# Optimization experiments

Measured on AMD Instinct MI355X. Metric: run time of the kernel, lower is better.

The kernel has to match this reference:

```python
import jax, jax.numpy as jnp
import numpy as np

N_FFT = 512
HOP = 256
HID = 512
VOCAB = 44
NB_BINS = 257  # n_fft//2 + 1, == max_bin
NEG = -100000.0
POS = 200000.0


def _hann(n):
    # torch.hann_window is periodic: 0.5*(1-cos(2*pi*k/N))
    return 0.5 * (1.0 - jnp.cos(2.0 * jnp.pi * jnp.arange(n, dtype=jnp.float32) / n))


def _stft_mag(x):
    # x: (B, C, T) -> (frames, B, C(mono=1), bins), magnitude spectrogram (power=1, mono mean)
    B, C, T = x.shape
    nfr = 1 + (T - N_FFT) // HOP
    idx = jnp.arange(nfr)[:, None] * HOP + jnp.arange(N_FFT)[None, :]
    frames = x.reshape(B * C, T)[:, idx] * _hann(N_FFT)      # (BC, F, n_fft)
    mag = jnp.abs(jnp.fft.rfft(frames, axis=-1))             # (BC, F, bins)
    mag = mag.reshape(B, C, nfr, N_FFT // 2 + 1).mean(axis=1, keepdims=True)
    return mag.transpose(2, 0, 1, 3)                          # (F, B, 1, bins)


def _lstm(x, wih, whh, b, reverse):
    # x: (T, B, in). torch gate order i, f, g, o. Returns hidden states (T, B, H).
    Bt, H = x.shape[1], whh.shape[1]
    def step(carry, xt):
        h, c = carry
        g = xt @ wih.T + h @ whh.T + b
        i, f, gg, o = jnp.split(g, 4, axis=-1)
        c = jax.nn.sigmoid(f) * c + jax.nn.sigmoid(i) * jnp.tanh(gg)
        h = jax.nn.sigmoid(o) * jnp.tanh(c)
        return (h, c), h
    init = (jnp.zeros((Bt, H), x.dtype), jnp.zeros((Bt, H), x.dtype))
    _, hs = jax.lax.scan(step, init, x, reverse=reverse)
    return hs


def _bilstm(x, wih, whh, b):
    # wih: (2, 4H, in) [fwd, bwd]
    hf = _lstm(x, wih[0], whh[0], b[0], False)
    hb = _lstm(x, wih[1], whh[1], b[1], True)
    return jnp.concatenate([hf, hb], axis=-1)


def _bn(x, g, b):
    # BatchNorm1d in training mode: batch statistics over axis 0, eps=1e-5
    mu = x.mean(0)
    v = ((x - mu) ** 2).mean(0)
    return g * (x - mu) * jax.lax.rsqrt(v + 1e-5) + b


def _dtw(scores):
    # dtw[n,m] = scores[n-1,m-1] + max(dtw[n-1,m], dtw[n-1,m-1]); row-wise scan
    B, N, M = scores.shape
    row0 = jnp.full((B, M + 1), NEG, scores.dtype).at[:, 0].set(POS)
    negcol = jnp.full((B, 1), NEG, scores.dtype)
    def step(prev, s):  # prev: (B, M+1), s: (B, M)
        shifted = jnp.concatenate([negcol, prev[:, :-1]], axis=1)
        new = jnp.concatenate([negcol, s + jnp.maximum(prev, shifted)[:, 1:]], axis=1)
        return new, new[:, 1:]
    _, rows = jax.lax.scan(step, row0, scores.transpose(1, 0, 2))  # (N, B, M)
    return rows.transpose(1, 0, 2)


def setup_inputs() -> dict:
    key = jax.random.key(0)
    ks = jax.random.split(key, 10)
    B, T, L = 8, 524544, 512
    s = 0.05
    H2 = HID // 2  # per-direction hidden = 256
    return {
        "x_audio": jax.random.normal(ks[0], (B, 1, T), jnp.float32),
        "text_idx": jax.random.randint(ks[1], (B, L), 0, VOCAB),
        "txt_wih": jax.random.normal(ks[2], (2, 4 * H2, VOCAB), jnp.float32) * s,
        "txt_whh": jax.random.normal(ks[3], (2, 4 * H2, H2), jnp.float32) * s,
        "txt_b": jax.random.normal(ks[4], (2, 4 * H2), jnp.float32) * s,
        "w_s": jax.random.normal(ks[5], (HID, HID), jnp.float32) / np.sqrt(HID).astype(np.float32),
        "fc1_w": jax.random.normal(ks[6], (HID, NB_BINS), jnp.float32) * s,
        "bn1_g": jnp.ones((HID,), jnp.float32),
        "bn1_b": jnp.zeros((HID,), jnp.float32),
        "input_mean": jnp.zeros((NB_BINS,), jnp.float32),
        "input_scale": jnp.ones((NB_BINS,), jnp.float32),
        "ae_wih": jax.random.normal(ks[7], (2, 2, 4 * H2, HID), jnp.float32) * s,
        "ae_whh": jax.random.normal(ks[8], (2, 2, 4 * H2, H2), jnp.float32) * s,
        "ae_b": jax.random.normal(ks[9], (2, 2, 4 * H2), jnp.float32) * s,
    }


def reference(x_audio, text_idx, txt_wih, txt_whh, txt_b, w_s, fc1_w, bn1_g, bn1_b,
              input_mean, input_scale, ae_wih, ae_whh, ae_b):
    mag = _stft_mag(x_audio)                 # (F, B, 1, bins)
    nfr, B, C, _ = mag.shape
    # text encoder (batch_first LSTM -> time-major internally)
    oneh = jax.nn.one_hot(text_idx, VOCAB, dtype=mag.dtype)           # (B, L, V)
    h = _bilstm(oneh.transpose(1, 0, 2), txt_wih, txt_whh, txt_b)     # (L, B, HID)
    h = h.transpose(1, 0, 2)                                          # (B, L, HID)
    # audio front-end
    x = (mag[..., :NB_BINS] + input_mean) * input_scale
    x = x.reshape(nfr * B, C * NB_BINS) @ fc1_w.T
    x = jnp.tanh(_bn(x, bn1_g, bn1_b)).reshape(nfr, B, HID)
    # 2-layer bidirectional audio encoder LSTM (dropout inactive / eval)
    for l in range(2):
        x = _bilstm(x, ae_wih[l], ae_whh[l], ae_b[l])
    x = x.transpose(1, 0, 2)                                          # (B, F, HID)
    side = jnp.einsum('hk,blk->bhl', w_s, h)                          # (B, HID, L)
    scores = jnp.einsum('bfh,bhl->bfl', x, side)                      # (B, F, L)
    return _dtw(scores)
```

## Files before the change

kernel.cpp:

```cpp
#include <hip/hip_runtime.h>
#include <hip/hip_bf16.h>

#define NFR    2048
#define BATCHN 8
#define NFFT   512
#define HOPSZ  256
#define BINS   257
#define HIDDEN 512
#define LTXT   512
#define TAUD   524544
#define NEGV  -100000.0f
#define POSV   200000.0f

using short8 = __attribute__((ext_vector_type(8))) short;
using u16x8  = __attribute__((ext_vector_type(8))) unsigned short;
using f32x4  = __attribute__((ext_vector_type(4))) float;
using int4v  = __attribute__((ext_vector_type(4))) int;

__device__ __forceinline__ unsigned short f2bf(float x) {
  union { float f; unsigned u; } v; v.f = x;
  unsigned u = v.u;
  u += 0x7fffu + ((u >> 16) & 1u);
  return (unsigned short)(u >> 16);
}
__device__ __forceinline__ float bf2f(unsigned short h) {
  union { unsigned u; float f; } v; v.u = ((unsigned)h) << 16;
  return v.f;
}

__device__ __forceinline__ float fsigm(float x) {
  return __builtin_amdgcn_rcpf(1.f + __expf(-x));
}
__device__ __forceinline__ float ftanh(float x) {
  return 2.f * __builtin_amdgcn_rcpf(1.f + __expf(-2.f * x)) - 1.f;
}

__device__ __forceinline__ size_t gin3_index(int t, int dir, int b, int gt, int u) {
  return (((size_t)t * 2 + dir) * 16 + (u >> 4)) * 512 +
         (size_t)((u & 15) * 32 + b * 4 + gt);
}

__global__ __launch_bounds__(256) void zero_kernel(int* p, int n) {
  int i = blockIdx.x * 256 + threadIdx.x;
  if (i < n) p[i] = 0;
}

__global__ __launch_bounds__(256) void stft_kernel(const float* __restrict__ x,
    const float* __restrict__ imean, const float* __restrict__ iscale,
    float* __restrict__ y)
{
  __shared__ float tab[512];
  __shared__ float xs[512];
  __shared__ float red[4];
  int f = blockIdx.x, b = blockIdx.y, tid = threadIdx.x;
  for (int m = tid; m < 512; m += 256)
    tab[m] = cosf(6.283185307179586e0f / 512.0f * (float)m);
  __syncthreads();
  const float* xb = x + (size_t)b * TAUD + (size_t)f * HOPSZ;
  for (int n = tid; n < 512; n += 256)
    xs[n] = xb[n] * 0.5f * (1.0f - tab[n]);
  __syncthreads();
  {
    int k = tid;
    float ar = 0.f, ai = 0.f;
    int m = 0;
    for (int n = 0; n < 512; ++n) {
      float xv = xs[n];
      ar += xv * tab[m];
      ai += xv * tab[(m + 384) & 511];
      m = (m + k) & 511;
    }
    float mag = sqrtf(ar * ar + ai * ai);
    y[((size_t)f * BATCHN + b) * BINS + k] = (mag + imean[k]) * iscale[k];
  }
  {
    float part = xs[2 * tid] - xs[2 * tid + 1];
#pragma unroll
    for (int o = 32; o; o >>= 1) part += __shfl_down(part, o, 64);
    if ((tid & 63) == 0) red[tid >> 6] = part;
    __syncthreads();
    if (tid == 0) {
      float s = red[0] + red[1] + red[2] + red[3];
      y[((size_t)f * BATCHN + b) * BINS + 256] =
          (fabsf(s) + imean[256]) * iscale[256];
    }
  }
}

__global__ __launch_bounds__(256) void transpose_kernel(const float* __restrict__ in,
    float* __restrict__ out, int R, int C, long inBatch, long outBatch)
{
  __shared__ float tile[32][33];
  const float* ib = in + (size_t)blockIdx.z * inBatch;
  float* ob = out + (size_t)blockIdx.z * outBatch;
  int r0 = blockIdx.y * 32, c0 = blockIdx.x * 32;
  int tx = threadIdx.x & 31, ty = threadIdx.x >> 5;
  for (int i = ty; i < 32; i += 8) {
    int r = r0 + i, c = c0 + tx;
    if (r < R && c < C) tile[i][tx] = ib[(size_t)r * C + c];
  }
  __syncthreads();
  for (int i = ty; i < 32; i += 8) {
    int c = c0 + i, r = r0 + tx;
    if (r < R && c < C) ob[(size_t)c * R + r] = tile[tx][i];
  }
}

__device__ __forceinline__ void storeval(float* p, float v) { *p = v; }
__device__ __forceinline__ void storeval(unsigned short* p, float v) { *p = f2bf(v); }

template <typename OutT>
__global__ __launch_bounds__(256) void gemm_kernel(
    const float* __restrict__ A, long lda, long strideA,
    const float* __restrict__ B, long ldb, long strideB,
    OutT* __restrict__ C, long ldc, long strideC,
    int K, const float* __restrict__ bias,
    const float* __restrict__ trA, const float* __restrict__ trB, int ginmode)
{
  __shared__ float As[16][512];
  int bz = blockIdx.z;
  A += (size_t)bz * strideA; B += (size_t)bz * strideB; C += (size_t)bz * strideC;
  int rowb = blockIdx.x * 16;
  int colb = blockIdx.y * 512;
  int tid = threadIdx.x;
  for (int r = 0; r < 16; ++r)
    for (int k = tid; k < K; k += 256) {
      float v = A[(size_t)(rowb + r) * lda + k];
      if (trA) v = tanhf(trA[k] * v + trB[k]);
      As[r][k] = v;
    }
  __syncthreads();
  float acc0[16], acc1[16];
#pragma unroll
  for (int r = 0; r < 16; ++r) { acc0[r] = 0.f; acc1[r] = 0.f; }
  int c0 = colb + tid, c1 = colb + tid + 256;
  for (int k = 0; k < K; ++k) {
    float b0 = B[(size_t)k * ldb + c0];
    float b1 = B[(size_t)k * ldb + c1];
#pragma unroll
    for (int r = 0; r < 16; ++r) {
      acc0[r] = fmaf(As[r][k], b0, acc0[r]);
      acc1[r] = fmaf(As[r][k], b1, acc1[r]);
    }
  }
  float bs0 = bias ? bias[c0] : 0.f;
  float bs1 = bias ? bias[c1] : 0.f;
  if (ginmode) {
    unsigned short* Cg = (unsigned short*)C;
    for (int r = 0; r < 16; ++r) {
      int row = rowb + r; int t = row >> 3; int b = row & 7;
      { int dir = c0 >> 10, j = c0 & 1023;
        Cg[gin3_index(t, dir, b, j >> 8, j & 255)] = f2bf(acc0[r] + bs0); }
      { int dir = c1 >> 10, j = c1 & 1023;
        Cg[gin3_index(t, dir, b, j >> 8, j & 255)] = f2bf(acc1[r] + bs1); }
    }
  } else {
    for (int r = 0; r < 16; ++r) {
      storeval(C + (size_t)(rowb + r) * ldc + c0, acc0[r] + bs0);
      storeval(C + (size_t)(rowb + r) * ldc + c1, acc1[r] + bs1);
    }
  }
}

__global__ __launch_bounds__(256) void bn_stats_kernel(const float* __restrict__ z,
                                                       float* __restrict__ stats)
{
  int rowb = blockIdx.x * 64;
  int c = threadIdx.x * 2;
  float s0 = 0, s1 = 0, q0 = 0, q1 = 0;
  for (int r = 0; r < 64; ++r) {
    const float* p = z + (size_t)(rowb + r) * 512 + c;
    float v0 = p[0], v1 = p[1];
    s0 += v0; s1 += v1; q0 += v0 * v0; q1 += v1 * v1;
  }
  atomicAdd(&stats[c], s0);       atomicAdd(&stats[c + 1], s1);
  atomicAdd(&stats[512 + c], q0); atomicAdd(&stats[512 + c + 1], q1);
}

__global__ void bn_fin_kernel(float* stats, const float* __restrict__ g,
                              const float* __restrict__ b)
{
  int h = threadIdx.x;
  float mu  = stats[h] * (1.0f / 16384.0f);
  float var = stats[512 + h] * (1.0f / 16384.0f) - mu * mu;
  float a = g[h] * rsqrtf(var + 1e-5f);
  stats[1024 + h] = a;
  stats[1536 + h] = b[h] - mu * a;
}

__global__ __launch_bounds__(256) void text_gin_kernel(const int* __restrict__ idx,
    const float* __restrict__ twT, const float* __restrict__ tb,
    unsigned short* __restrict__ gin3t)
{
  size_t i = (size_t)blockIdx.x * 256 + threadIdx.x;
  if (i >= (size_t)LTXT * 8 * 2048) return;
  int j   = i & 1023;
  int dir = (i >> 10) & 1;
  int b   = (i >> 11) & 7;
  int l   = (int)(i >> 14);
  int v = idx[b * 512 + l];
  float val = twT[((size_t)dir * 44 + v) * 1024 + j] + tb[dir * 1024 + j];
  gin3t[gin3_index(l, dir, b, j >> 8, j & 255)] = f2bf(val);
}

__global__ __launch_bounds__(1024) void lstm_kernel(
    const unsigned short* __restrict__ gA, const float* __restrict__ whA,
    float* __restrict__ outA, long ostTA, long ostBA, int TA,
    const unsigned short* __restrict__ gB, const float* __restrict__ whB,
    float* __restrict__ outB, long ostTB, long ostBB, int TB)
{
  __shared__ unsigned char hlds[2][16][256];
  __shared__ int redis[16][4][33][4];
  int job = blockIdx.x >> 1, dir = blockIdx.x & 1;
  const unsigned short* gin3 = job ? gB : gA;
  const float* whh = job ? whB : whA;
  float* out = job ? outB : outA;
  long ostT = job ? ostTB : ostTA;
  long ostB = job ? ostBB : ostBA;
  int T = job ? TB : TA;

  int tid = threadIdx.x;
  int w = tid >> 6;
  int lane = tid & 63;
  int col = lane & 15, lg = lane >> 4;

  int4v fb[4][4];
  {
    const float* wb = whh + (size_t)dir * 1024 * 256;
#pragma unroll
    for (int gt = 0; gt < 4; ++gt) {
      const float* wr = wb + (size_t)(gt * 256 + w * 16 + col) * 256 + lg * 16;
#pragma unroll
      for (int cc = 0; cc < 4; ++cc) {
        const float* p = wr + cc * 64;
        int4v v;
#pragma unroll
        for (int e = 0; e < 4; ++e) {
          unsigned wd = 0;
#pragma unroll
          for (int by = 0; by < 4; ++by) {
            float q = rintf(p[e * 4 + by] * 256.f);
            q = fminf(fmaxf(q, -127.f), 127.f);
            wd |= ((unsigned)((int)q & 255)) << (8 * by);
          }
          v[e] = (int)wd;
        }
        fb[gt][cc] = v;
      }
    }
  }

  {
    int* hz = (int*)hlds;
    for (int i = tid; i < 2048; i += 1024) hz[i] = 0;
  }
  __syncthreads();

  float cst0 = 0.f, cst1 = 0.f;
  int b0 = 2 * lg, b1 = 2 * lg + 1;
  int u = w * 16 + col;
  const float invS = 1.f / (256.f * 127.f);
  int r0i = (2 * lg) & 3;
  int l32r = col + (lg >> 1) * 16;

  const unsigned short* glane = gin3 + (size_t)dir * 8192 + (size_t)w * 512 +
                                (size_t)(col * 32 + lg * 8);

  u16x8 grA, grB;
  {
    int t0 = dir ? (T - 1) : 0;
    int t1 = dir ? (T - 2) : 1;
    grA = *(const u16x8*)(glane + (size_t)t0 * 16384);
    grB = *(const u16x8*)(glane + (size_t)t1 * 16384);
  }

  auto step = [&](int s, u16x8& gr) {
    int t = dir ? (T - 1 - s) : s;
    int p = s & 1;

    int4v fa[4];
#pragma unroll
    for (int cc = 0; cc < 4; ++cc) {
      int off = col * 256 + (((cc * 64) + lg * 16) ^ ((col & 7) << 4));
      fa[cc] = *(const int4v*)((const char*)&hlds[p][0][0] + off);
    }

    int4v acc[4];
#pragma unroll
    for (int gt = 0; gt < 4; ++gt) { int4v z = {0, 0, 0, 0}; acc[gt] = z; }
#pragma unroll
    for (int cc = 0; cc < 4; ++cc) {
#pragma unroll
      for (int gt = 0; gt < 4; ++gt) {
        acc[gt] = __builtin_amdgcn_mfma_i32_16x16x64_i8(fa[cc], fb[gt][cc],
                                                        acc[gt], 0, 0, 0);
      }
    }

    if (lg < 2) {
#pragma unroll
      for (int r = 0; r < 4; ++r) {
        int4v tv; tv[0] = acc[0][r]; tv[1] = acc[1][r];
        tv[2] = acc[2][r]; tv[3] = acc[3][r];
        *(int4v*)&redis[w][r][col + lg * 16][0] = tv;
      }
    }
    int4v ga = *(const int4v*)&redis[w][r0i][l32r][0];
    int4v gb = *(const int4v*)&redis[w][r0i + 1][l32r][0];

    float g0[4], g1[4];
#pragma unroll
    for (int gt = 0; gt < 4; ++gt) {
      g0[gt] = bf2f(gr[gt])     + (float)ga[gt] * invS;
      g1[gt] = bf2f(gr[4 + gt]) + (float)gb[gt] * invS;
    }

    float gi0 = fsigm(g0[0]), gf0 = fsigm(g0[1]), gg0 = ftanh(g0[2]), go0 = fsigm(g0[3]);
    float gi1 = fsigm(g1[0]), gf1 = fsigm(g1[1]), gg1 = ftanh(g1[2]), go1 = fsigm(g1[3]);
    float c0 = gf0 * cst0 + gi0 * gg0; cst0 = c0;
    float c1 = gf1 * cst1 + gi1 * gg1; cst1 = c1;
    float h0 = go0 * ftanh(c0);
    float h1 = go1 * ftanh(c1);

    out[(size_t)t * ostT + (size_t)b0 * ostB + dir * 256 + u] = h0;
    out[(size_t)t * ostT + (size_t)b1 * ostB + dir * 256 + u] = h1;
    hlds[p ^ 1][b0][u ^ ((b0 & 7) << 4)] = (unsigned char)(int)rintf(h0 * 127.f);
    hlds[p ^ 1][b1][u ^ ((b1 & 7) << 4)] = (unsigned char)(int)rintf(h1 * 127.f);

    if (s + 2 < T) {
      int tn = dir ? (T - 3 - s) : (s + 2);
      gr = *(const u16x8*)(glane + (size_t)tn * 16384);
    }
    __syncthreads();
  };

  for (int s = 0; s < T; s += 2) {
    step(s, grA);
    step(s + 1, grB);
  }
}

__global__ __launch_bounds__(256) void dtw_kernel(float* __restrict__ sc)
{
  __shared__ float P[513];
  int b = blockIdx.x, tid = threadIdx.x;
  for (int j = tid; j < 513; j += 256) P[j] = (j == 0) ? POSV : NEGV;
  __syncthreads();
  float* base = sc + (size_t)b * NFR * 512;
  float s0 = base[tid], s1 = base[tid + 256];
  for (int n = 0; n < NFR; ++n) {
    float* row = base + (size_t)n * 512;
    float t0 = s0, t1 = s1;
    if (n + 1 < NFR) { s0 = row[512 + tid]; s1 = row[768 + tid]; }
    float v0 = t0 + fmaxf(P[tid + 1], P[tid]);
    float v1 = t1 + fmaxf(P[tid + 257], P[tid + 256]);
    __syncthreads();
    P[tid + 1] = v0; P[tid + 257] = v1;
    if (tid == 0) P[0] = NEGV;
    row[tid] = v0; row[tid + 256] = v1;
    __syncthreads();
  }
}

extern "C" void kernel_launch(void* const* d_in, const int* in_sizes, int n_in,
                              void* d_out, int out_size, void* d_ws, size_t ws_size,
                              hipStream_t stream) {
  const float* x_audio  = (const float*)d_in[0];
  const int*   text_idx = (const int*)d_in[1];
  const float* txt_wih  = (const float*)d_in[2];
  const float* txt_whh  = (const float*)d_in[3];
  const float* txt_b    = (const float*)d_in[4];
  const float* w_s      = (const float*)d_in[5];
  const float* fc1_w    = (const float*)d_in[6];
  const float* bn1_g    = (const float*)d_in[7];
  const float* bn1_b    = (const float*)d_in[8];
  const float* imean    = (const float*)d_in[9];
  const float* iscale   = (const float*)d_in[10];
  const float* ae_wih   = (const float*)d_in[11];
  const float* ae_whh   = (const float*)d_in[12];
  const float* ae_b     = (const float*)d_in[13];

  char* ws = (char*)d_ws;
  size_t off = 0;
  auto alloc = [&](size_t sz) { size_t o = off; off += (sz + 255) & ~255ull; return o; };
  size_t OFF_Y    = alloc(16384ull * 257 * 4);
  size_t OFF_WT   = alloc(257ull * 512 * 4);
  size_t OFF_TWT  = alloc(2ull * 44 * 1024 * 4);
  size_t OFF_WIHT = alloc(512ull * 2048 * 4);
  size_t OFF_Z    = alloc(16384ull * 512 * 4);
  size_t OFF_L1   = alloc(16384ull * 512 * 4);
  size_t OFF_L2   = alloc(16384ull * 512 * 4);
  size_t OFF_TXT  = alloc(8ull * 512 * 512 * 4);
  size_t OFF_GIN  = alloc(16384ull * 2048 * 2);
  size_t OFF_HTT  = OFF_GIN;
  size_t OFF_SIDE = OFF_GIN + 8ull * 512 * 512 * 4;
  size_t OFF_STATS = alloc(2048ull * 4);
  (void)ws_size; (void)in_sizes; (void)n_in; (void)out_size;

  float* y       = (float*)(ws + OFF_Y);
  float* wT      = (float*)(ws + OFF_WT);
  float* twT     = (float*)(ws + OFF_TWT);
  float* wihT    = (float*)(ws + OFF_WIHT);
  float* z       = (float*)(ws + OFF_Z);
  float* l1out   = (float*)(ws + OFF_L1);
  float* l2out   = (float*)(ws + OFF_L2);
  float* textout = (float*)(ws + OFF_TXT);
  unsigned short* gin3a = (unsigned short*)(ws + OFF_GIN);
  unsigned short* gin3t = (unsigned short*)(ws + OFF_L2);
  float* htT     = (float*)(ws + OFF_HTT);
  float* side    = (float*)(ws + OFF_SIDE);
  float* stats   = (float*)(ws + OFF_STATS);
  float* outp = (float*)d_out;

  zero_kernel<<<8, 256, 0, stream>>>((int*)(ws + OFF_STATS), 2048);

  stft_kernel<<<dim3(NFR, BATCHN), 256, 0, stream>>>(x_audio, imean, iscale, y);

  transpose_kernel<<<dim3(9, 16, 1), 256, 0, stream>>>(fc1_w, wT, 512, 257, 0, 0);
  transpose_kernel<<<dim3(2, 32, 2), 256, 0, stream>>>(txt_wih, twT, 1024, 44,
                                                       1024 * 44, 44 * 1024);

  gemm_kernel<float><<<dim3(1024, 1, 1), 256, 0, stream>>>(
      y, 257, 0, wT, 512, 0, z, 512, 0, 257, nullptr, nullptr, nullptr, 0);
  bn_stats_kernel<<<256, 256, 0, stream>>>(z, stats);
  bn_fin_kernel<<<1, 512, 0, stream>>>(stats, bn1_g, bn1_b);

  text_gin_kernel<<<32768, 256, 0, stream>>>(text_idx, twT, txt_b, gin3t);

  transpose_kernel<<<dim3(16, 64, 1), 256, 0, stream>>>(ae_wih, wihT, 2048, 512, 0, 0);
  gemm_kernel<unsigned short><<<dim3(1024, 4, 1), 256, 0, stream>>>(
      z, 512, 0, wihT, 2048, 0, gin3a, 0, 0, 512, ae_b,
      stats + 1024, stats + 1536, 1);

  lstm_kernel<<<4, 1024, 0, stream>>>(
      gin3a, ae_whh, l1out, 4096, 512, NFR,
      gin3t, txt_whh, textout, 512, 512 * 512, LTXT);

  transpose_kernel<<<dim3(16, 64, 1), 256, 0, stream>>>(
      ae_wih + 2ull * 1024 * 512, wihT, 2048, 512, 0, 0);
  gemm_kernel<unsigned short><<<dim3(1024, 4, 1), 256, 0, stream>>>(
      l1out, 512, 0, wihT, 2048, 0, gin3a, 0, 0, 512, ae_b + 2048,
      nullptr, nullptr, 1);

  lstm_kernel<<<2, 1024, 0, stream>>>(
      gin3a, ae_whh + 2ull * 1024 * 256, l2out, 4096, 512, NFR,
      gin3a, ae_whh + 2ull * 1024 * 256, l2out, 4096, 512, NFR);

  transpose_kernel<<<dim3(16, 16, 8), 256, 0, stream>>>(textout, htT, 512, 512,
                                                        512 * 512, 512 * 512);
  gemm_kernel<float><<<dim3(32, 1, 8), 256, 0, stream>>>(
      w_s, 512, 0, htT, 512, 512 * 512, side, 512, 512 * 512, 512,
      nullptr, nullptr, nullptr, 0);

  gemm_kernel<float><<<dim3(128, 1, 8), 256, 0, stream>>>(
      l2out, 4096, 512, side, 512, 512 * 512, outp, 512, (long)NFR * 512, 512,
      nullptr, nullptr, nullptr, 0);
  dtw_kernel<<<8, 256, 0, stream>>>(outp);
}
```

Measured before the change: 9.203 ms.

## Halve LSTM block size, use permlane32 swap instead of LDS gate redistribution

```diff
diff --git a/kernel.cpp b/kernel.cpp
--- a/kernel.cpp
+++ b/kernel.cpp
@@ -35,9 +35,10 @@
   return 2.f * __builtin_amdgcn_rcpf(1.f + __expf(-2.f * x)) - 1.f;
 }
 
-__device__ __forceinline__ size_t gin3_index(int t, int dir, int b, int gt, int u) {
-  return (((size_t)t * 2 + dir) * 16 + (u >> 4)) * 512 +
-         (size_t)((u & 15) * 32 + b * 4 + gt);
+__device__ __forceinline__ size_t gin5_index(int t, int dir, int b, int gt, int u) {
+  int w = u >> 5, ul = u & 31, bgrp = b >> 2, br = b & 3;
+  return (((size_t)t * 2 + dir) * 8 + w) * 1024 +
+         (size_t)((bgrp * 32 + ul) * 16 + br * 4 + gt);
 }
 
 __global__ __launch_bounds__(256) void zero_kernel(int* p, int n) {
@@ -150,9 +151,9 @@
     for (int r = 0; r < 16; ++r) {
       int row = rowb + r; int t = row >> 3; int b = row & 7;
       { int dir = c0 >> 10, j = c0 & 1023;
-        Cg[gin3_index(t, dir, b, j >> 8, j & 255)] = f2bf(acc0[r] + bs0); }
+        Cg[gin5_index(t, dir, b, j >> 8, j & 255)] = f2bf(acc0[r] + bs0); }
       { int dir = c1 >> 10, j = c1 & 1023;
-        Cg[gin3_index(t, dir, b, j >> 8, j & 255)] = f2bf(acc1[r] + bs1); }
+        Cg[gin5_index(t, dir, b, j >> 8, j & 255)] = f2bf(acc1[r] + bs1); }
     }
   } else {
     for (int r = 0; r < 16; ++r) {
@@ -190,7 +191,7 @@
 
 __global__ __launch_bounds__(256) void text_gin_kernel(const int* __restrict__ idx,
     const float* __restrict__ twT, const float* __restrict__ tb,
-    unsigned short* __restrict__ gin3t)
+    unsigned short* __restrict__ gin5t)
 {
   size_t i = (size_t)blockIdx.x * 256 + threadIdx.x;
   if (i >= (size_t)LTXT * 8 * 2048) return;
@@ -200,19 +201,59 @@
   int l   = (int)(i >> 14);
   int v = idx[b * 512 + l];
   float val = twT[((size_t)dir * 44 + v) * 1024 + j] + tb[dir * 1024 + j];
-  gin3t[gin3_index(l, dir, b, j >> 8, j & 255)] = f2bf(val);
-}
-
-__global__ __launch_bounds__(1024) void lstm_kernel(
+  gin5t[gin5_index(l, dir, b, j >> 8, j & 255)] = f2bf(val);
+}
+
+#define LSTM_STEP(P, gv0, gv1)                                                  \
+  {                                                                             \
+    int4v fa[4];                                                                \
+    _Pragma("unroll")                                                           \
+    for (int cc = 0; cc < 4; ++cc) {                                            \
+      int off = col * 256 + (((cc * 64) + lg * 16) ^ ((col & 7) << 4));         \
+      fa[cc] = *(const int4v*)((const char*)&hlds[P][0][0] + off);              \
+    }                                                                           \
+    int4v acc[8];                                                               \
+    _Pragma("unroll")                                                           \
+    for (int n = 0; n < 8; ++n) { int4v z = {0, 0, 0, 0}; acc[n] = z; }         \
+    _Pragma("unroll")                                                           \
+    for (int cc = 0; cc < 4; ++cc) {                                            \
+      _Pragma("unroll")                                                         \
+      for (int n = 0; n < 8; ++n)                                               \
+        acc[n] = __builtin_amdgcn_mfma_i32_16x16x64_i8(fa[cc], fb[n][cc],       \
+                                                       acc[n], 0, 0, 0);        \
+    }                                                                           \
+    _Pragma("unroll")                                                           \
+    for (int r = 0; r < 4; ++r) {                                               \
+      float g[4];                                                               \
+      _Pragma("unroll")                                                         \
+      for (int gt = 0; gt < 4; ++gt) {                                          \
+        int av = acc[gt * 2][r], bv = acc[gt * 2 + 1][r];                       \
+        asm("v_permlane32_swap_b32 %0, %1" : "+v"(av), "+v"(bv));               \
+        unsigned short gu = (r < 2) ? (gv0)[(r & 1) * 4 + gt]                   \
+                                    : (gv1)[(r & 1) * 4 + gt];                  \
+        g[gt] = fmaf((float)av, invS, bf2f(gu));                                \
+      }                                                                         \
+      float si = fsigm(g[0]), sf = fsigm(g[1]);                                 \
+      float tg = ftanh(g[2]), so = fsigm(g[3]);                                 \
+      float c = sf * cst[r] + si * tg; cst[r] = c;                              \
+      float h = so * ftanh(c);                                                  \
+      *ob[r] = h; ob[r] += tstep;                                               \
+      int q = (int)rintf(h * 127.f);                                            \
+      int b = bbase + r;                                                        \
+      hlds[(P) ^ 1][b][u ^ ((b & 7) << 4)] = (unsigned char)q;                  \
+    }                                                                           \
+    __syncthreads();                                                            \
+  }
+
+__global__ __launch_bounds__(512) void lstm_kernel(
     const unsigned short* __restrict__ gA, const float* __restrict__ whA,
     float* __restrict__ outA, long ostTA, long ostBA, int TA,
     const unsigned short* __restrict__ gB, const float* __restrict__ whB,
     float* __restrict__ outB, long ostTB, long ostBB, int TB)
 {
   __shared__ unsigned char hlds[2][16][256];
-  __shared__ int redis[16][4][33][4];
   int job = blockIdx.x >> 1, dir = blockIdx.x & 1;
-  const unsigned short* gin3 = job ? gB : gA;
+  const unsigned short* gin = job ? gB : gA;
   const float* whh = job ? whB : whA;
   float* out = job ? outB : outA;
   long ostT = job ? ostTB : ostTA;
@@ -224,12 +265,13 @@
   int lane = tid & 63;
   int col = lane & 15, lg = lane >> 4;
 
-  int4v fb[4][4];
+  int4v fb[8][4];
   {
     const float* wb = whh + (size_t)dir * 1024 * 256;
 #pragma unroll
-    for (int gt = 0; gt < 4; ++gt) {
-      const float* wr = wb + (size_t)(gt * 256 + w * 16 + col) * 256 + lg * 16;
+    for (int n = 0; n < 8; ++n) {
+      int gt = n >> 1, uh = n & 1;
+      const float* wr = wb + (size_t)(gt * 256 + w * 32 + uh * 16 + col) * 256 + lg * 16;
 #pragma unroll
       for (int cc = 0; cc < 4; ++cc) {
         const float* p = wr + cc * 64;
@@ -245,98 +287,47 @@
           }
           v[e] = (int)wd;
         }
-        fb[gt][cc] = v;
+        fb[n][cc] = v;
       }
     }
   }
 
   {
     int* hz = (int*)hlds;
-    for (int i = tid; i < 2048; i += 1024) hz[i] = 0;
-  }
-  __syncthreads();
-
-  float cst0 = 0.f, cst1 = 0.f;
-  int b0 = 2 * lg, b1 = 2 * lg + 1;
-  int u = w * 16 + col;
+    for (int i = tid; i < 2048; i += 512) hz[i] = 0;
+  }
+  __syncthreads();
+
   const float invS = 1.f / (256.f * 127.f);
-  int r0i = (2 * lg) & 3;
-  int l32r = col + (lg >> 1) * 16;
-
-  const unsigned short* glane = gin3 + (size_t)dir * 8192 + (size_t)w * 512 +
-                                (size_t)(col * 32 + lg * 8);
-
-  u16x8 grA, grB;
+  float cst[4] = {0.f, 0.f, 0.f, 0.f};
+  int u = w * 32 + (lg >> 1) * 16 + col;
+  int bbase = (lg & 1) * 4;
+
+  long tstep = dir ? -ostT : ostT;
+  float* ob[4];
   {
     int t0 = dir ? (T - 1) : 0;
-    int t1 = dir ? (T - 2) : 1;
-    grA = *(const u16x8*)(glane + (size_t)t0 * 16384);
-    grB = *(const u16x8*)(glane + (size_t)t1 * 16384);
-  }
-
-  auto step = [&](int s, u16x8& gr) {
-    int t = dir ? (T - 1 - s) : s;
-    int p = s & 1;
-
-    int4v fa[4];
-#pragma unroll
-    for (int cc = 0; cc < 4; ++cc) {
-      int off = col * 256 + (((cc * 64) + lg * 16) ^ ((col & 7) << 4));
-      fa[cc] = *(const int4v*)((const char*)&hlds[p][0][0] + off);
-    }
-
-    int4v acc[4];
-#pragma unroll
-    for (int gt = 0; gt < 4; ++gt) { int4v z = {0, 0, 0, 0}; acc[gt] = z; }
-#pragma unroll
-    for (int cc = 0; cc < 4; ++cc) {
-#pragma unroll
-      for (int gt = 0; gt < 4; ++gt) {
-        acc[gt] = __builtin_amdgcn_mfma_i32_16x16x64_i8(fa[cc], fb[gt][cc],
-                                                        acc[gt], 0, 0, 0);
-      }
-    }
-
-    if (lg < 2) {
-#pragma unroll
-      for (int r = 0; r < 4; ++r) {
-        int4v tv; tv[0] = acc[0][r]; tv[1] = acc[1][r];
-        tv[2] = acc[2][r]; tv[3] = acc[3][r];
-        *(int4v*)&redis[w][r][col + lg * 16][0] = tv;
-      }
-    }
-    int4v ga = *(const int4v*)&redis[w][r0i][l32r][0];
-    int4v gb = *(const int4v*)&redis[w][r0i + 1][l32r][0];
-
-    float g0[4], g1[4];
-#pragma unroll
-    for (int gt = 0; gt < 4; ++gt) {
-      g0[gt] = bf2f(gr[gt])     + (float)ga[gt] * invS;
-      g1[gt] = bf2f(gr[4 + gt]) + (float)gb[gt] * invS;
-    }
-
-    float gi0 = fsigm(g0[0]), gf0 = fsigm(g0[1]), gg0 = ftanh(g0[2]), go0 = fsigm(g0[3]);
-    float gi1 = fsigm(g1[0]), gf1 = fsigm(g1[1]), gg1 = ftanh(g1[2]), go1 = fsigm(g1[3]);
-    float c0 = gf0 * cst0 + gi0 * gg0; cst0 = c0;
-    float c1 = gf1 * cst1 + gi1 * gg1; cst1 = c1;
-    float h0 = go0 * ftanh(c0);
-    float h1 = go1 * ftanh(c1);
-
-    out[(size_t)t * ostT + (size_t)b0 * ostB + dir * 256 + u] = h0;
-    out[(size_t)t * ostT + (size_t)b1 * ostB + dir * 256 + u] = h1;
-    hlds[p ^ 1][b0][u ^ ((b0 & 7) << 4)] = (unsigned char)(int)rintf(h0 * 127.f);
-    hlds[p ^ 1][b1][u ^ ((b1 & 7) << 4)] = (unsigned char)(int)rintf(h1 * 127.f);
-
-    if (s + 2 < T) {
-      int tn = dir ? (T - 3 - s) : (s + 2);
-      gr = *(const u16x8*)(glane + (size_t)tn * 16384);
-    }
-    __syncthreads();
-  };
+    float* o = out + (size_t)t0 * ostT + dir * 256 + u;
+#pragma unroll
+    for (int r = 0; r < 4; ++r) ob[r] = o + (size_t)(bbase + r) * ostB;
+  }
+
+  const unsigned short* glane = gin + (size_t)dir * 8192 + (size_t)w * 1024 +
+      (size_t)(((lg & 1) * 32 + (lg >> 1) * 16 + col) * 16);
+  long gstep2 = (dir ? -2l : 2l) * 16384;
+  const unsigned short* gpA = glane + (size_t)(dir ? (T - 1) : 0) * 16384;
+  const unsigned short* gpB = glane + (size_t)(dir ? (T - 2) : 1) * 16384;
+  u16x8 grA0 = *(const u16x8*)gpA, grA1 = *(const u16x8*)(gpA + 8);
+  u16x8 grB0 = *(const u16x8*)gpB, grB1 = *(const u16x8*)(gpB + 8);
+  gpA += gstep2; gpB += gstep2;
 
   for (int s = 0; s < T; s += 2) {
-    step(s, grA);
-    step(s + 1, grB);
+    u16x8 nA0 = *(const u16x8*)gpA, nA1 = *(const u16x8*)(gpA + 8);
+    u16x8 nB0 = *(const u16x8*)gpB, nB1 = *(const u16x8*)(gpB + 8);
+    gpA += gstep2; gpB += gstep2;
+    LSTM_STEP(0, grA0, grA1)
+    LSTM_STEP(1, grB0, grB1)
+    grA0 = nA0; grA1 = nA1; grB0 = nB0; grB1 = nB1;
   }
 }
 
@@ -394,8 +385,9 @@
   size_t OFF_GIN  = alloc(16384ull * 2048 * 2);
   size_t OFF_HTT  = OFF_GIN;
   size_t OFF_SIDE = OFF_GIN + 8ull * 512 * 512 * 4;
+  size_t OFF_PAD  = alloc(262144);
   size_t OFF_STATS = alloc(2048ull * 4);
-  (void)ws_size; (void)in_sizes; (void)n_in; (void)out_size;
+  (void)ws_size; (void)in_sizes; (void)n_in; (void)out_size; (void)OFF_PAD;
 
   float* y       = (float*)(ws + OFF_Y);
   float* wT      = (float*)(ws + OFF_WT);
@@ -405,8 +397,8 @@
   float* l1out   = (float*)(ws + OFF_L1);
   float* l2out   = (float*)(ws + OFF_L2);
   float* textout = (float*)(ws + OFF_TXT);
-  unsigned short* gin3a = (unsigned short*)(ws + OFF_GIN);
-  unsigned short* gin3t = (unsigned short*)(ws + OFF_L2);
+  unsigned short* gin5a = (unsigned short*)(ws + OFF_GIN);
+  unsigned short* gin5t = (unsigned short*)(ws + OFF_L2);
   float* htT     = (float*)(ws + OFF_HTT);
   float* side    = (float*)(ws + OFF_SIDE);
   float* stats   = (float*)(ws + OFF_STATS);
@@ -425,26 +417,26 @@
   bn_stats_kernel<<<256, 256, 0, stream>>>(z, stats);
   bn_fin_kernel<<<1, 512, 0, stream>>>(stats, bn1_g, bn1_b);
 
-  text_gin_kernel<<<32768, 256, 0, stream>>>(text_idx, twT, txt_b, gin3t);
+  text_gin_kernel<<<32768, 256, 0, stream>>>(text_idx, twT, txt_b, gin5t);
 
   transpose_kernel<<<dim3(16, 64, 1), 256, 0, stream>>>(ae_wih, wihT, 2048, 512, 0, 0);
   gemm_kernel<unsigned short><<<dim3(1024, 4, 1), 256, 0, stream>>>(
-      z, 512, 0, wihT, 2048, 0, gin3a, 0, 0, 512, ae_b,
+      z, 512, 0, wihT, 2048, 0, gin5a, 0, 0, 512, ae_b,
       stats + 1024, stats + 1536, 1);
 
-  lstm_kernel<<<4, 1024, 0, stream>>>(
-      gin3a, ae_whh, l1out, 4096, 512, NFR,
-      gin3t, txt_whh, textout, 512, 512 * 512, LTXT);
+  lstm_kernel<<<4, 512, 0, stream>>>(
+      gin5a, ae_whh, l1out, 4096, 512, NFR,
+      gin5t, txt_whh, textout, 512, 512 * 512, LTXT);
 
   transpose_kernel<<<dim3(16, 64, 1), 256, 0, stream>>>(
       ae_wih + 2ull * 1024 * 512, wihT, 2048, 512, 0, 0);
   gemm_kernel<unsigned short><<<dim3(1024, 4, 1), 256, 0, stream>>>(
-      l1out, 512, 0, wihT, 2048, 0, gin3a, 0, 0, 512, ae_b + 2048,
+      l1out, 512, 0, wihT, 2048, 0, gin5a, 0, 0, 512, ae_b + 2048,
       nullptr, nullptr, 1);
 
-  lstm_kernel<<<2, 1024, 0, stream>>>(
-      gin3a, ae_whh + 2ull * 1024 * 256, l2out, 4096, 512, NFR,
-      gin3a, ae_whh + 2ull * 1024 * 256, l2out, 4096, 512, NFR);
+  lstm_kernel<<<2, 512, 0, stream>>>(
+      gin5a, ae_whh + 2ull * 1024 * 256, l2out, 4096, 512, NFR,
+      gin5a, ae_whh + 2ull * 1024 * 256, l2out, 4096, 512, NFR);
 
   transpose_kernel<<<dim3(16, 16, 8), 256, 0, stream>>>(textout, htT, 512, 512,
                                                         512 * 512, 512 * 512);
```

Result: faster. 8.595 ms (-6.6%).
